# Kernel tuning notes

Hardware: AMD Instinct MI355X
Metric: run time of the kernel (lower is better)

The kernel has to match this reference:

```python
import jax, jax.numpy as jnp
import numpy as np

N_NODES = 100000
N_EDGES = 400000
N_GRAPHS = 4000
IN_DIM = 128
HID = 512
N_DESC = 200
N_CLASSES = 2


def setup_inputs() -> dict:
    key = jax.random.key(0)
    ks = jax.random.split(key, 16)
    features = jax.random.normal(ks[0], (N_NODES, IN_DIM), jnp.float32)
    descriptors = jax.random.normal(ks[1], (N_GRAPHS, N_DESC), jnp.float32)
    src = jax.random.randint(ks[2], (N_EDGES,), 0, N_NODES)
    dst = jax.random.randint(ks[3], (N_EDGES,), 0, N_NODES)
    node2graph = jnp.sort(jax.random.randint(ks[4], (N_NODES,), 0, N_GRAPHS))

    def unif(k, shape, fan_out):
        stdv = 1.0 / np.sqrt(fan_out)
        return jax.random.uniform(k, shape, jnp.float32, -stdv, stdv)

    # GCN layer params (torch init: uniform(-1/sqrt(out), 1/sqrt(out)))
    W1 = unif(ks[5], (IN_DIM, HID), HID)
    b1 = unif(ks[6], (HID,), HID)
    W2 = unif(ks[7], (HID, HID), HID)
    b2 = unif(ks[8], (HID,), HID)
    # MLP head (torch Linear default init: uniform(-1/sqrt(fan_in), ...))
    lw1 = unif(ks[9], (HID + N_DESC, 500), HID + N_DESC)
    lb1 = unif(ks[10], (500,), HID + N_DESC)
    lw2 = unif(ks[11], (500, 100), 500)
    lb2 = unif(ks[12], (100,), 500)
    cw = unif(ks[13], (100, N_CLASSES), 100)
    cb = unif(ks[14], (N_CLASSES,), 100)
    return {"features": features, "descriptors": descriptors, "src": src,
            "dst": dst, "node2graph": node2graph, "W1": W1, "b1": b1,
            "W2": W2, "b2": b2, "lw1": lw1, "lb1": lb1, "lw2": lw2,
            "lb2": lb2, "cw": cw, "cb": cb}


def reference(features, descriptors, src, dst, node2graph,
              W1, b1, W2, b2, lw1, lb1, lw2, lb2, cw, cb):
    N = features.shape[0]
    B = descriptors.shape[0]

    def gcn(h, W, b):
        hW = h @ W                                    # [N, F_out]
        # copy_src + sum: gather source features per edge, scatter-sum to dst
        agg = jax.ops.segment_sum(hW[src], dst, num_segments=N)
        return jax.nn.relu(agg + b)

    h = gcn(features, W1, b1)                         # dropout skipped (eval)
    h = gcn(h, W2, b2)

    # dgl.mean_nodes: per-graph mean over nodes
    sums = jax.ops.segment_sum(h, node2graph, num_segments=B)     # [B, HID]
    counts = jax.ops.segment_sum(jnp.ones((N,), h.dtype), node2graph,
                                 num_segments=B)
    hg = sums / jnp.maximum(counts, 1.0)[:, None]

    x = jnp.concatenate([hg, descriptors], axis=1)    # [B, HID+N_DESC]
    x = jax.nn.relu(x @ lw1 + lb1)
    x = jax.nn.relu(x @ lw2 + lb2)
    return x @ cw + cb                                # [B, n_classes]
```

## Files before the change

kernel.cpp:

```cpp
#include <hip/hip_runtime.h>
#include <hip/hip_bf16.h>

#define N_NODES  100000
#define N_EDGES  400000
#define N_GRAPHS 4000
#define IN_DIM   128
#define HID      512
#define N_DESC   200
#define N_CLASSES 2
#define MLP1_OUT 500
#define MLP2_OUT 100
#define XIN_DIM  (HID + N_DESC)
#define XIN_PAD  768

#define SCAN_CHUNK 1024
#define NCHK ((N_NODES + SCAN_CHUNK - 1) / SCAN_CHUNK)

typedef __hip_bfloat16  bf16;
typedef __hip_bfloat162 bf16x2;
typedef short s8v  __attribute__((ext_vector_type(8)));
typedef float f32x4 __attribute__((ext_vector_type(4)));

__device__ __forceinline__ float ldf(const float* p, size_t i) { return p[i]; }
__device__ __forceinline__ float ldf(const bf16* p, size_t i)  { return __bfloat162float(p[i]); }

__device__ __forceinline__ float2 ld2(const float* p, int i) { return ((const float2*)p)[i]; }
__device__ __forceinline__ float2 ld2(const bf16* p, int i)  {
    return __bfloat1622float2(((const bf16x2*)p)[i]);
}

__device__ __forceinline__ void store_out(float* p, float v) { *p = v; }
__device__ __forceinline__ void store_out(bf16* p, float v)  { *p = __float2bfloat16(v); }

__device__ __forceinline__ short f2bs(float x) {
    bf16 h = __float2bfloat16(x);
    return __builtin_bit_cast(short, h);
}

__device__ __forceinline__ void gld16(const short* g, short* l) {
    __builtin_amdgcn_global_load_lds(
        (const __attribute__((address_space(1))) unsigned int*)g,
        (__attribute__((address_space(3))) unsigned int*)l, 16, 0, 0);
}

__global__ __launch_bounds__(256)
void detect_dtype_kernel(const unsigned* __restrict__ words, unsigned nw,
                         int* __restrict__ flag)
{
    __shared__ int s_cnt;
    if (threadIdx.x == 0) s_cnt = 0;
    __syncthreads();
    const int SAMPLES = 2048;
    int sane = 0;
    for (int i = threadIdx.x; i < SAMPLES; i += 256) {
        size_t idx = (size_t)(((unsigned long long)i * 2654435761ull) % nw);
        unsigned w = words[idx];
        float f = __uint_as_float((w & 0xFFFFu) << 16);
        float a = fabsf(f);
        if (f == 0.0f || (a > 1e-8f && a < 1e8f)) sane++;
    }
    atomicAdd(&s_cnt, sane);
    __syncthreads();
    if (threadIdx.x == 0) *flag = (s_cnt * 10 > SAMPLES * 6) ? 1 : 0;
}

template<typename FT, int MODE>
__global__ __launch_bounds__(256)
void prep_weights_kernel(const FT* __restrict__ W1, const FT* __restrict__ W2,
                         const FT* __restrict__ lw1, const FT* __restrict__ lw2,
                         const FT* __restrict__ b1, const FT* __restrict__ b2,
                         const FT* __restrict__ lb1, const FT* __restrict__ lb2,
                         short* __restrict__ W1t, short* __restrict__ W2t,
                         short* __restrict__ lw1t, short* __restrict__ lw2t,
                         float* __restrict__ b1f, float* __restrict__ b2f,
                         float* __restrict__ lb1f, float* __restrict__ lb2f,
                         const int* __restrict__ flag)
{
    if (*flag != MODE) return;
    int i = blockIdx.x * 256 + threadIdx.x;
    if (i < 65536) {
        int n = i >> 7, k = i & 127;
        W1t[i] = f2bs(ldf(W1, (size_t)k * HID + n));
        return;
    }
    i -= 65536;
    if (i < 262144) {
        int n = i >> 9, k = i & 511;
        W2t[i] = f2bs(ldf(W2, (size_t)k * HID + n));
        return;
    }
    i -= 262144;
    if (i < 393216) {
        int n = i / XIN_PAD, k = i - n * XIN_PAD;
        lw1t[i] = (n < MLP1_OUT && k < XIN_DIM)
                      ? f2bs(ldf(lw1, (size_t)k * MLP1_OUT + n)) : (short)0;
        return;
    }
    i -= 393216;
    if (i < 65536) {
        int n = i >> 9, k = i & 511;
        lw2t[i] = (n < MLP2_OUT && k < MLP1_OUT)
                      ? f2bs(ldf(lw2, (size_t)k * MLP2_OUT + n)) : (short)0;
        return;
    }
    i -= 65536;
    if (i < 512) { b1f[i] = ldf(b1, i); return; }
    i -= 512;
    if (i < 512) { b2f[i] = ldf(b2, i); return; }
    i -= 512;
    if (i < 512) { lb1f[i] = (i < MLP1_OUT) ? ldf(lb1, i) : 0.f; return; }
    i -= 512;
    if (i < 128) { lb2f[i] = (i < MLP2_OUT) ? ldf(lb2, i) : 0.f; return; }
}

__global__ __launch_bounds__(256)
void deg_kernel(const int* __restrict__ dst, int* __restrict__ deg)
{
    int e = blockIdx.x * 256 + threadIdx.x;
    if (e < N_EDGES) atomicAdd(&deg[dst[e]], 1);
}

__global__ __launch_bounds__(256)
void scan_partial_kernel(const int* __restrict__ deg, int* __restrict__ part)
{
    int c = blockIdx.x, t = threadIdx.x;
    int i0 = c * SCAN_CHUNK + t * 4;
    int s = 0;
#pragma unroll
    for (int j = 0; j < 4; j++) {
        int i = i0 + j;
        if (i < N_NODES) s += deg[i];
    }
    __shared__ int red[256];
    red[t] = s;
    __syncthreads();
    for (int off = 128; off > 0; off >>= 1) {
        if (t < off) red[t] += red[t + off];
        __syncthreads();
    }
    if (t == 0) part[c] = red[0];
}

__global__ void scan_parts_kernel(int* __restrict__ part, int* __restrict__ edge_start)
{
    int run = 0;
    for (int c = 0; c < NCHK; c++) { int v = part[c]; part[c] = run; run += v; }
    edge_start[N_NODES] = run;
}

__global__ __launch_bounds__(256)
void scan_final_kernel(const int* __restrict__ deg, const int* __restrict__ part,
                       int* __restrict__ edge_start, int* __restrict__ cursor)
{
    int c = blockIdx.x, t = threadIdx.x;
    int i0 = c * SCAN_CHUNK + t * 4;
    int d[4];
    int tsum = 0;
#pragma unroll
    for (int j = 0; j < 4; j++) {
        int i = i0 + j;
        d[j] = (i < N_NODES) ? deg[i] : 0;
        tsum += d[j];
    }
    __shared__ int s[256];
    s[t] = tsum;
    __syncthreads();
    for (int off = 1; off < 256; off <<= 1) {
        int v = (t >= off) ? s[t - off] : 0;
        __syncthreads();
        s[t] += v;
        __syncthreads();
    }
    int run = part[c] + s[t] - tsum;
#pragma unroll
    for (int j = 0; j < 4; j++) {
        int i = i0 + j;
        if (i < N_NODES) { edge_start[i] = run; cursor[i] = run; run += d[j]; }
    }
}

__global__ __launch_bounds__(256)
void fill_kernel(const int* __restrict__ src, const int* __restrict__ dst,
                 int* __restrict__ cursor, int* __restrict__ csr_src)
{
    int e = blockIdx.x * 256 + threadIdx.x;
    if (e >= N_EDGES) return;
    int p = atomicAdd(&cursor[dst[e]], 1);
    csr_src[p] = src[e];
}

__global__ __launch_bounds__(256)
void gstart_kernel(const int* __restrict__ n2g, int* __restrict__ gstart)
{
    int n = blockIdx.x * 256 + threadIdx.x;
    if (n > N_NODES) return;
    if (n == N_NODES) {
        int last = n2g[N_NODES - 1];
        for (int g = last + 1; g <= N_GRAPHS; g++) gstart[g] = N_NODES;
        return;
    }
    int v = n2g[n];
    int prev = (n == 0) ? -1 : n2g[n - 1];
    for (int g = prev + 1; g <= v; g++) gstart[g] = n;
}

template<typename FT, int MODE>
__global__ __launch_bounds__(256)
void gather_feat_kernel(const FT* __restrict__ feat, const int* __restrict__ edge_start,
                        const int* __restrict__ csr_src, bf16* __restrict__ agg1,
                        const int* __restrict__ flag)
{
    if (*flag != MODE) return;
    int n = blockIdx.x * 4 + (threadIdx.x >> 6);
    if (n >= N_NODES) return;
    int lane = threadIdx.x & 63;
    int e0 = edge_start[n], e1 = edge_start[n + 1];
    float2 acc = {0.f, 0.f};
    for (int i = e0; i < e1; i++) {
        int s = csr_src[i];
        float2 f = ld2(feat + (size_t)s * IN_DIM, lane);
        acc.x += f.x; acc.y += f.y;
    }
    bf16x2 p;
    p.x = __float2bfloat16(acc.x);
    p.y = __float2bfloat16(acc.y);
    ((bf16x2*)(agg1 + (size_t)n * IN_DIM))[lane] = p;
}

__global__ __launch_bounds__(256)
void gather_h_kernel(const bf16* __restrict__ h1, const int* __restrict__ edge_start,
                     const int* __restrict__ csr_src, bf16* __restrict__ aggc)
{
    int n = blockIdx.x * 4 + (threadIdx.x >> 6);
    if (n >= N_NODES) return;
    int lane = threadIdx.x & 63;
    int e0 = edge_start[n], e1 = edge_start[n + 1];
    float acc[8];
#pragma unroll
    for (int j = 0; j < 8; j++) acc[j] = 0.f;
    for (int i = e0; i < e1; i++) {
        int s = csr_src[i];
        float4 r = ((const float4*)(h1 + (size_t)s * HID))[lane];
        const bf16x2* p = (const bf16x2*)&r;
#pragma unroll
        for (int q = 0; q < 4; q++) {
            float2 f = __bfloat1622float2(p[q]);
            acc[2 * q] += f.x; acc[2 * q + 1] += f.y;
        }
    }
    s8v s;
#pragma unroll
    for (int j = 0; j < 8; j++) s[j] = f2bs(acc[j]);
    ((float4*)(aggc + (size_t)n * HID))[lane] = __builtin_bit_cast(float4, s);
}

template<int NCT>
__global__ __launch_bounds__(256)
void mfma_gemm_kernel(const short* __restrict__ A, const short* __restrict__ Bt,
                      const float* __restrict__ biasf, bf16* __restrict__ Cout,
                      int M, int K, int nrt)
{
    __shared__ short smem[17408];
    short* As = smem;
    short* Bs = smem + 8192;
    short* Cs = smem;

    const int b  = blockIdx.x;
    const int r8 = b & 7;
    const int t  = b >> 3;
    const int x  = (t / NCT) * 8 + r8;
    const int y  = t % NCT;
    if (x >= nrt) return;
    const int row0 = x * 128;
    const int col0 = y * 128;

    const int tid  = threadIdx.x;
    const int lane = tid & 63;
    const int w    = tid >> 6;
    const int wr = w >> 1, wc = w & 1;
    const int m  = lane & 15, q = lane >> 4;

    const int dr = lane >> 3;
    const int dc = ((lane & 7) ^ dr) * 8;
    const short* ga[4];
    const short* gb[4];
    short* la[4];
    short* lb[4];
#pragma unroll
    for (int c = 0; c < 4; c++) {
        int r = (w * 4 + c) * 8 + dr;
        ga[c] = A  + (size_t)(row0 + r) * K + dc;
        gb[c] = Bt + (size_t)(col0 + r) * K + dc;
        la[c] = As + (w * 4 + c) * 512;
        lb[c] = Bs + (w * 4 + c) * 512;
    }

    const int sa = ((q ^ (m & 7)) * 8);

    f32x4 acc[4][4];
#pragma unroll
    for (int i = 0; i < 4; i++)
#pragma unroll
        for (int j = 0; j < 4; j++) acc[i][j] = {0.f, 0.f, 0.f, 0.f};

    for (int k0 = 0; k0 < K; k0 += 64) {
#pragma unroll
        for (int c = 0; c < 4; c++) gld16(ga[c], la[c]);
#pragma unroll
        for (int c = 0; c < 4; c++) gld16(gb[c], lb[c]);
#pragma unroll
        for (int c = 0; c < 4; c++) { ga[c] += 64; gb[c] += 64; }
        __syncthreads();

#pragma unroll
        for (int kq = 0; kq < 2; kq++) {
            const int so = sa ^ (kq * 32);
            s8v av[4], bv[4];
#pragma unroll
            for (int rt = 0; rt < 4; rt++)
                av[rt] = *(const s8v*)&As[(wr * 64 + rt * 16 + m) * 64 + so];
#pragma unroll
            for (int ct = 0; ct < 4; ct++)
                bv[ct] = *(const s8v*)&Bs[(wc * 64 + ct * 16 + m) * 64 + so];
#pragma unroll
            for (int rt = 0; rt < 4; rt++)
#pragma unroll
                for (int ct = 0; ct < 4; ct++)
                    acc[rt][ct] = __builtin_amdgcn_mfma_f32_16x16x32_bf16(
                        av[rt], bv[ct], acc[rt][ct], 0, 0, 0);
        }
        __syncthreads();
    }

#pragma unroll
    for (int rt = 0; rt < 4; rt++) {
#pragma unroll
        for (int ct = 0; ct < 4; ct++) {
            int lcol = wc * 64 + ct * 16 + m;
            float bv = biasf[col0 + lcol];
#pragma unroll
            for (int reg = 0; reg < 4; reg++) {
                int lrow = wr * 64 + rt * 16 + q * 4 + reg;
                float v = acc[rt][ct][reg] + bv;
                v = v > 0.f ? v : 0.f;
                Cs[lrow * 136 + lcol] = f2bs(v);
            }
        }
    }
    __syncthreads();

#pragma unroll
    for (int it = 0; it < 8; it++) {
        int idx = it * 256 + tid;
        int r = idx >> 4;
        int c = (idx & 15) * 8;
        int row = row0 + r;
        if (row < M)
            *(float4*)&Cout[(size_t)row * HID + col0 + c] =
                *(const float4*)&Cs[r * 136 + c];
    }
}

__global__ __launch_bounds__(256)
void pool_graph_kernel(const bf16* __restrict__ h2, const int* __restrict__ gstart,
                       float* __restrict__ hg)
{
    int g = blockIdx.x * 4 + (threadIdx.x >> 6);
    if (g >= N_GRAPHS) return;
    int lane = threadIdx.x & 63;
    int s0 = gstart[g], s1 = gstart[g + 1];
    float acc[8];
#pragma unroll
    for (int j = 0; j < 8; j++) acc[j] = 0.f;
    for (int n = s0; n < s1; n++) {
        float4 r = ((const float4*)(h2 + (size_t)n * HID))[lane];
        const bf16x2* p = (const bf16x2*)&r;
#pragma unroll
        for (int q = 0; q < 4; q++) {
            float2 f = __bfloat1622float2(p[q]);
            acc[2 * q] += f.x; acc[2 * q + 1] += f.y;
        }
    }
    float* orow = hg + (size_t)g * HID + lane * 8;
    ((float4*)orow)[0] = make_float4(acc[0], acc[1], acc[2], acc[3]);
    ((float4*)orow)[1] = make_float4(acc[4], acc[5], acc[6], acc[7]);
}

template<typename FT, int MODE>
__global__ __launch_bounds__(256)
void build_xin_kernel(const float* __restrict__ hg, const int* __restrict__ gstart,
                      const FT* __restrict__ desc, bf16* __restrict__ xinb,
                      const int* __restrict__ flag)
{
    if (*flag != MODE) return;
    int idx = blockIdx.x * 256 + threadIdx.x;
    if (idx >= N_GRAPHS * XIN_PAD) return;
    int g = idx / XIN_PAD;
    int c = idx - g * XIN_PAD;
    float v;
    if (c < HID) {
        float cnt = (float)(gstart[g + 1] - gstart[g]);
        v = hg[(size_t)g * HID + c] / (cnt > 1.0f ? cnt : 1.0f);
    } else if (c < XIN_DIM) {
        v = ldf(desc, (size_t)g * N_DESC + (c - HID));
    } else {
        v = 0.f;
    }
    xinb[idx] = __float2bfloat16(v);
}

template<typename FT, int MODE>
__global__ __launch_bounds__(256)
void final_layer_kernel(const bf16* __restrict__ x2b, const FT* __restrict__ cw,
                        const FT* __restrict__ cb, FT* __restrict__ out,
                        const int* __restrict__ flag)
{
    if (*flag != MODE) return;
    int i = blockIdx.x * 256 + threadIdx.x;
    if (i >= N_GRAPHS * N_CLASSES) return;
    int r = i >> 1, c = i & 1;
    float acc = ldf(cb, c);
    const bf16* x = x2b + (size_t)r * HID;
#pragma unroll 4
    for (int k = 0; k < MLP2_OUT; k++)
        acc += __bfloat162float(x[k]) * ldf(cw, k * N_CLASSES + c);
    store_out(&out[i], acc);
}

static inline size_t align_up(size_t x, size_t a) { return (x + a - 1) & ~(a - 1); }
static inline int swgrid(int nrt, int nct) { return ((nrt + 7) / 8) * 8 * nct; }

extern "C" void kernel_launch(void* const* d_in, const int* in_sizes, int n_in,
                              void* d_out, int out_size, void* d_ws, size_t ws_size,
                              hipStream_t stream)
{
    const void* features    = d_in[0];
    const void* descriptors = d_in[1];
    const int*  src         = (const int*)d_in[2];
    const int*  dst         = (const int*)d_in[3];
    const int*  node2graph  = (const int*)d_in[4];
    const void* W1          = d_in[5];
    const void* b1          = d_in[6];
    const void* W2          = d_in[7];
    const void* b2          = d_in[8];
    const void* lw1         = d_in[9];
    const void* lb1         = d_in[10];
    const void* lw2         = d_in[11];
    const void* lb2         = d_in[12];
    const void* cw          = d_in[13];
    const void* cb          = d_in[14];
    (void)in_sizes; (void)n_in; (void)out_size; (void)ws_size;

    char* ws = (char*)d_ws;
    size_t off = 0;
    bf16* agg1 = (bf16*)(ws + off);
    bf16* aggc = (bf16*)(ws + off);
    bf16* xinb = (bf16*)(ws + off);
    bf16* x1b  = (bf16*)(ws + off + (size_t)8 * 1024 * 1024);
    bf16* x2b  = (bf16*)(ws + off + (size_t)16 * 1024 * 1024);
    off = align_up(off + (size_t)N_NODES * HID * sizeof(bf16), 256);
    bf16* h1 = (bf16*)(ws + off);
    bf16* h2 = (bf16*)(ws + off);
    off = align_up(off + (size_t)N_NODES * HID * sizeof(bf16), 256);
    float* hg = (float*)(ws + off);
    off = align_up(off + (size_t)N_GRAPHS * HID * sizeof(float), 256);
    int* dflag = (int*)(ws + off);          off = align_up(off + 256, 256);
    int* edge_start = (int*)(ws + off);     off = align_up(off + (N_NODES + 1) * 4, 256);
    int* cursor = (int*)(ws + off);         off = align_up(off + N_NODES * 4, 256);
    int* csr_src = (int*)(ws + off);        off = align_up(off + N_EDGES * 4, 256);
    int* part = (int*)(ws + off);           off = align_up(off + NCHK * 4, 256);
    int* deg = (int*)(ws + off);            off = align_up(off + N_NODES * 4, 256);
    int* gstart = (int*)(ws + off);         off = align_up(off + (N_GRAPHS + 1) * 4, 256);
    short* W1t  = (short*)(ws + off);       off = align_up(off + (size_t)HID * IN_DIM * 2, 256);
    short* W2t  = (short*)(ws + off);       off = align_up(off + (size_t)HID * HID * 2, 256);
    short* lw1t = (short*)(ws + off);       off = align_up(off + (size_t)512 * XIN_PAD * 2, 256);
    short* lw2t = (short*)(ws + off);       off = align_up(off + (size_t)128 * HID * 2, 256);
    float* b1f  = (float*)(ws + off);       off = align_up(off + 512 * 4, 256);
    float* b2f  = (float*)(ws + off);       off = align_up(off + 512 * 4, 256);
    float* lb1f = (float*)(ws + off);       off = align_up(off + 512 * 4, 256);
    float* lb2f = (float*)(ws + off);       off = align_up(off + 128 * 4, 256);

    detect_dtype_kernel<<<1, 256, 0, stream>>>(
        (const unsigned*)features, (unsigned)(N_NODES * IN_DIM / 2), dflag);

    {
        int nblk = (788096 + 255) / 256;
        prep_weights_kernel<float, 0><<<nblk, 256, 0, stream>>>(
            (const float*)W1, (const float*)W2, (const float*)lw1, (const float*)lw2,
            (const float*)b1, (const float*)b2, (const float*)lb1, (const float*)lb2,
            W1t, W2t, lw1t, lw2t, b1f, b2f, lb1f, lb2f, dflag);
        prep_weights_kernel<bf16, 1><<<nblk, 256, 0, stream>>>(
            (const bf16*)W1, (const bf16*)W2, (const bf16*)lw1, (const bf16*)lw2,
            (const bf16*)b1, (const bf16*)b2, (const bf16*)lb1, (const bf16*)lb2,
            W1t, W2t, lw1t, lw2t, b1f, b2f, lb1f, lb2f, dflag);
    }

    hipMemsetAsync(deg, 0, N_NODES * 4, stream);
    deg_kernel<<<(N_EDGES + 255) / 256, 256, 0, stream>>>(dst, deg);
    scan_partial_kernel<<<NCHK, 256, 0, stream>>>(deg, part);
    scan_parts_kernel<<<1, 1, 0, stream>>>(part, edge_start);
    scan_final_kernel<<<NCHK, 256, 0, stream>>>(deg, part, edge_start, cursor);
    fill_kernel<<<(N_EDGES + 255) / 256, 256, 0, stream>>>(src, dst, cursor, csr_src);
    gstart_kernel<<<(N_NODES + 256) / 256, 256, 0, stream>>>(node2graph, gstart);

    gather_feat_kernel<float, 0><<<N_NODES / 4, 256, 0, stream>>>(
        (const float*)features, edge_start, csr_src, agg1, dflag);
    gather_feat_kernel<bf16, 1><<<N_NODES / 4, 256, 0, stream>>>(
        (const bf16*)features, edge_start, csr_src, agg1, dflag);
    {
        int nrt = (N_NODES + 127) / 128;
        mfma_gemm_kernel<4><<<swgrid(nrt, 4), 256, 0, stream>>>(
            (const short*)agg1, W1t, b1f, h1, N_NODES, IN_DIM, nrt);
    }

    gather_h_kernel<<<N_NODES / 4, 256, 0, stream>>>(h1, edge_start, csr_src, aggc);
    {
        int nrt = (N_NODES + 127) / 128;
        mfma_gemm_kernel<4><<<swgrid(nrt, 4), 256, 0, stream>>>(
            (const short*)aggc, W2t, b2f, h2, N_NODES, HID, nrt);
    }
    pool_graph_kernel<<<N_GRAPHS / 4, 256, 0, stream>>>(h2, gstart, hg);

    {
        int nthr = (N_GRAPHS * XIN_PAD + 255) / 256;
        build_xin_kernel<float, 0><<<nthr, 256, 0, stream>>>(
            hg, gstart, (const float*)descriptors, xinb, dflag);
        build_xin_kernel<bf16, 1><<<nthr, 256, 0, stream>>>(
            hg, gstart, (const bf16*)descriptors, xinb, dflag);
    }
    {
        int nrt = (N_GRAPHS + 127) / 128;
        mfma_gemm_kernel<4><<<swgrid(nrt, 4), 256, 0, stream>>>(
            (const short*)xinb, lw1t, lb1f, x1b, N_GRAPHS, XIN_PAD, nrt);
    }
    {
        int nrt = (N_GRAPHS + 127) / 128;
        mfma_gemm_kernel<1><<<swgrid(nrt, 1), 256, 0, stream>>>(
            (const short*)x1b, lw2t, lb2f, x2b, N_GRAPHS, HID, nrt);
    }
    {
        int nthr = (N_GRAPHS * N_CLASSES + 255) / 256;
        final_layer_kernel<float, 0><<<nthr, 256, 0, stream>>>(
            x2b, (const float*)cw, (const float*)cb, (float*)d_out, dflag);
        final_layer_kernel<bf16, 1><<<nthr, 256, 0, stream>>>(
            x2b, (const bf16*)cw, (const bf16*)cb, (bf16*)d_out, dflag);
    }
}
```

Measured before the change: 478.5 us.

## Merge dtype-dispatched kernel pairs, unroll gathers by four, shrink GEMM epilogue LDS

Each pair of float/bf16 kernel launches gated by a device flag becomes a single launch that branches on the flag inside the kernel. This removes four redundant launches that did nothing but exit early. The edge gathers and graph pooling loops are unrolled by four so several independent row loads are in flight per wavefront. The GEMM epilogue now writes the output tile through LDS in two 64-row halves, which cuts shared memory to 16384 shorts and may raise occupancy, at the cost of an extra barrier.

```diff
diff --git a/kernel.cpp b/kernel.cpp
--- a/kernel.cpp
+++ b/kernel.cpp
@@ -29,9 +29,6 @@
     return __bfloat1622float2(((const bf16x2*)p)[i]);
 }
 
-__device__ __forceinline__ void store_out(float* p, float v) { *p = v; }
-__device__ __forceinline__ void store_out(bf16* p, float v)  { *p = __float2bfloat16(v); }
-
 __device__ __forceinline__ short f2bs(float x) {
     bf16 h = __float2bfloat16(x);
     return __builtin_bit_cast(short, h);
@@ -64,53 +61,55 @@
     if (threadIdx.x == 0) *flag = (s_cnt * 10 > SAMPLES * 6) ? 1 : 0;
 }
 
-template<typename FT, int MODE>
-__global__ __launch_bounds__(256)
-void prep_weights_kernel(const FT* __restrict__ W1, const FT* __restrict__ W2,
-                         const FT* __restrict__ lw1, const FT* __restrict__ lw2,
-                         const FT* __restrict__ b1, const FT* __restrict__ b2,
-                         const FT* __restrict__ lb1, const FT* __restrict__ lb2,
+__global__ __launch_bounds__(256)
+void prep_weights_kernel(const void* __restrict__ W1, const void* __restrict__ W2,
+                         const void* __restrict__ lw1, const void* __restrict__ lw2,
+                         const void* __restrict__ b1, const void* __restrict__ b2,
+                         const void* __restrict__ lb1, const void* __restrict__ lb2,
                          short* __restrict__ W1t, short* __restrict__ W2t,
                          short* __restrict__ lw1t, short* __restrict__ lw2t,
                          float* __restrict__ b1f, float* __restrict__ b2f,
                          float* __restrict__ lb1f, float* __restrict__ lb2f,
                          const int* __restrict__ flag)
 {
-    if (*flag != MODE) return;
+    const int bf = *flag;
+    auto rd = [&](const void* p, size_t idx) -> float {
+        return bf ? __bfloat162float(((const bf16*)p)[idx]) : ((const float*)p)[idx];
+    };
     int i = blockIdx.x * 256 + threadIdx.x;
     if (i < 65536) {
         int n = i >> 7, k = i & 127;
-        W1t[i] = f2bs(ldf(W1, (size_t)k * HID + n));
+        W1t[i] = f2bs(rd(W1, (size_t)k * HID + n));
         return;
     }
     i -= 65536;
     if (i < 262144) {
         int n = i >> 9, k = i & 511;
-        W2t[i] = f2bs(ldf(W2, (size_t)k * HID + n));
+        W2t[i] = f2bs(rd(W2, (size_t)k * HID + n));
         return;
     }
     i -= 262144;
     if (i < 393216) {
         int n = i / XIN_PAD, k = i - n * XIN_PAD;
         lw1t[i] = (n < MLP1_OUT && k < XIN_DIM)
-                      ? f2bs(ldf(lw1, (size_t)k * MLP1_OUT + n)) : (short)0;
+                      ? f2bs(rd(lw1, (size_t)k * MLP1_OUT + n)) : (short)0;
         return;
     }
     i -= 393216;
     if (i < 65536) {
         int n = i >> 9, k = i & 511;
         lw2t[i] = (n < MLP2_OUT && k < MLP1_OUT)
-                      ? f2bs(ldf(lw2, (size_t)k * MLP2_OUT + n)) : (short)0;
+                      ? f2bs(rd(lw2, (size_t)k * MLP2_OUT + n)) : (short)0;
         return;
     }
     i -= 65536;
-    if (i < 512) { b1f[i] = ldf(b1, i); return; }
+    if (i < 512) { b1f[i] = rd(b1, i); return; }
     i -= 512;
-    if (i < 512) { b2f[i] = ldf(b2, i); return; }
+    if (i < 512) { b2f[i] = rd(b2, i); return; }
     i -= 512;
-    if (i < 512) { lb1f[i] = (i < MLP1_OUT) ? ldf(lb1, i) : 0.f; return; }
+    if (i < 512) { lb1f[i] = (i < MLP1_OUT) ? rd(lb1, i) : 0.f; return; }
     i -= 512;
-    if (i < 128) { lb2f[i] = (i < MLP2_OUT) ? ldf(lb2, i) : 0.f; return; }
+    if (i < 128) { lb2f[i] = (i < MLP2_OUT) ? rd(lb2, i) : 0.f; return; }
 }
 
 __global__ __launch_bounds__(256)
@@ -204,19 +203,29 @@
     for (int g = prev + 1; g <= v; g++) gstart[g] = n;
 }
 
-template<typename FT, int MODE>
-__global__ __launch_bounds__(256)
-void gather_feat_kernel(const FT* __restrict__ feat, const int* __restrict__ edge_start,
-                        const int* __restrict__ csr_src, bf16* __restrict__ agg1,
-                        const int* __restrict__ flag)
-{
-    if (*flag != MODE) return;
+template<typename FT>
+__device__ __forceinline__ void gather_feat_body(const FT* __restrict__ feat,
+                                                 const int* __restrict__ edge_start,
+                                                 const int* __restrict__ csr_src,
+                                                 bf16* __restrict__ agg1)
+{
     int n = blockIdx.x * 4 + (threadIdx.x >> 6);
     if (n >= N_NODES) return;
     int lane = threadIdx.x & 63;
     int e0 = edge_start[n], e1 = edge_start[n + 1];
     float2 acc = {0.f, 0.f};
-    for (int i = e0; i < e1; i++) {
+    int i = e0;
+    for (; i + 4 <= e1; i += 4) {
+        int s0 = csr_src[i], s1 = csr_src[i + 1];
+        int s2 = csr_src[i + 2], s3 = csr_src[i + 3];
+        float2 f0 = ld2(feat + (size_t)s0 * IN_DIM, lane);
+        float2 f1 = ld2(feat + (size_t)s1 * IN_DIM, lane);
+        float2 f2 = ld2(feat + (size_t)s2 * IN_DIM, lane);
+        float2 f3 = ld2(feat + (size_t)s3 * IN_DIM, lane);
+        acc.x += (f0.x + f1.x) + (f2.x + f3.x);
+        acc.y += (f0.y + f1.y) + (f2.y + f3.y);
+    }
+    for (; i < e1; i++) {
         int s = csr_src[i];
         float2 f = ld2(feat + (size_t)s * IN_DIM, lane);
         acc.x += f.x; acc.y += f.y;
@@ -225,6 +234,25 @@
     p.x = __float2bfloat16(acc.x);
     p.y = __float2bfloat16(acc.y);
     ((bf16x2*)(agg1 + (size_t)n * IN_DIM))[lane] = p;
+}
+
+__global__ __launch_bounds__(256)
+void gather_feat_kernel(const void* __restrict__ feat, const int* __restrict__ edge_start,
+                        const int* __restrict__ csr_src, bf16* __restrict__ agg1,
+                        const int* __restrict__ flag)
+{
+    if (*flag) gather_feat_body((const bf16*)feat, edge_start, csr_src, agg1);
+    else       gather_feat_body((const float*)feat, edge_start, csr_src, agg1);
+}
+
+__device__ __forceinline__ void acc8(float* acc, float4 r)
+{
+    const bf16x2* p = (const bf16x2*)&r;
+#pragma unroll
+    for (int q = 0; q < 4; q++) {
+        float2 f = __bfloat1622float2(p[q]);
+        acc[2 * q] += f.x; acc[2 * q + 1] += f.y;
+    }
 }
 
 __global__ __launch_bounds__(256)
@@ -238,15 +266,19 @@
     float acc[8];
 #pragma unroll
     for (int j = 0; j < 8; j++) acc[j] = 0.f;
-    for (int i = e0; i < e1; i++) {
+    int i = e0;
+    for (; i + 4 <= e1; i += 4) {
+        int s0 = csr_src[i], s1 = csr_src[i + 1];
+        int s2 = csr_src[i + 2], s3 = csr_src[i + 3];
+        float4 r0 = ((const float4*)(h1 + (size_t)s0 * HID))[lane];
+        float4 r1 = ((const float4*)(h1 + (size_t)s1 * HID))[lane];
+        float4 r2 = ((const float4*)(h1 + (size_t)s2 * HID))[lane];
+        float4 r3 = ((const float4*)(h1 + (size_t)s3 * HID))[lane];
+        acc8(acc, r0); acc8(acc, r1); acc8(acc, r2); acc8(acc, r3);
+    }
+    for (; i < e1; i++) {
         int s = csr_src[i];
-        float4 r = ((const float4*)(h1 + (size_t)s * HID))[lane];
-        const bf16x2* p = (const bf16x2*)&r;
-#pragma unroll
-        for (int q = 0; q < 4; q++) {
-            float2 f = __bfloat1622float2(p[q]);
-            acc[2 * q] += f.x; acc[2 * q + 1] += f.y;
-        }
+        acc8(acc, ((const float4*)(h1 + (size_t)s * HID))[lane]);
     }
     s8v s;
 #pragma unroll
@@ -260,7 +292,7 @@
                       const float* __restrict__ biasf, bf16* __restrict__ Cout,
                       int M, int K, int nrt)
 {
-    __shared__ short smem[17408];
+    __shared__ short smem[16384];
     short* As = smem;
     short* Bs = smem + 8192;
     short* Cs = smem;
@@ -333,31 +365,36 @@
     }
 
 #pragma unroll
-    for (int rt = 0; rt < 4; rt++) {
-#pragma unroll
-        for (int ct = 0; ct < 4; ct++) {
-            int lcol = wc * 64 + ct * 16 + m;
-            float bv = biasf[col0 + lcol];
-#pragma unroll
-            for (int reg = 0; reg < 4; reg++) {
-                int lrow = wr * 64 + rt * 16 + q * 4 + reg;
-                float v = acc[rt][ct][reg] + bv;
-                v = v > 0.f ? v : 0.f;
-                Cs[lrow * 136 + lcol] = f2bs(v);
+    for (int half = 0; half < 2; half++) {
+        if (half == 1) __syncthreads();
+        if (wr == half) {
+#pragma unroll
+            for (int rt = 0; rt < 4; rt++) {
+#pragma unroll
+                for (int ct = 0; ct < 4; ct++) {
+                    int lcol = wc * 64 + ct * 16 + m;
+                    float bv = biasf[col0 + lcol];
+#pragma unroll
+                    for (int reg = 0; reg < 4; reg++) {
+                        int lrow = rt * 16 + q * 4 + reg;
+                        float v = acc[rt][ct][reg] + bv;
+                        v = v > 0.f ? v : 0.f;
+                        Cs[lrow * 136 + lcol] = f2bs(v);
+                    }
+                }
             }
         }
-    }
-    __syncthreads();
-
-#pragma unroll
-    for (int it = 0; it < 8; it++) {
-        int idx = it * 256 + tid;
-        int r = idx >> 4;
-        int c = (idx & 15) * 8;
-        int row = row0 + r;
-        if (row < M)
-            *(float4*)&Cout[(size_t)row * HID + col0 + c] =
-                *(const float4*)&Cs[r * 136 + c];
+        __syncthreads();
+#pragma unroll
+        for (int it = 0; it < 4; it++) {
+            int idx = it * 256 + tid;
+            int r = idx >> 4;
+            int c = (idx & 15) * 8;
+            int row = row0 + half * 64 + r;
+            if (row < M)
+                *(float4*)&Cout[(size_t)row * HID + col0 + c] =
+                    *(const float4*)&Cs[r * 136 + c];
+        }
     }
 }
 
@@ -372,27 +409,27 @@
     float acc[8];
 #pragma unroll
     for (int j = 0; j < 8; j++) acc[j] = 0.f;
-    for (int n = s0; n < s1; n++) {
-        float4 r = ((const float4*)(h2 + (size_t)n * HID))[lane];
-        const bf16x2* p = (const bf16x2*)&r;
-#pragma unroll
-        for (int q = 0; q < 4; q++) {
-            float2 f = __bfloat1622float2(p[q]);
-            acc[2 * q] += f.x; acc[2 * q + 1] += f.y;
-        }
-    }
+    int n = s0;
+    for (; n + 4 <= s1; n += 4) {
+        float4 r0 = ((const float4*)(h2 + (size_t)(n + 0) * HID))[lane];
+        float4 r1 = ((const float4*)(h2 + (size_t)(n + 1) * HID))[lane];
+        float4 r2 = ((const float4*)(h2 + (size_t)(n + 2) * HID))[lane];
+        float4 r3 = ((const float4*)(h2 + (size_t)(n + 3) * HID))[lane];
+        acc8(acc, r0); acc8(acc, r1); acc8(acc, r2); acc8(acc, r3);
+    }
+    for (; n < s1; n++)
+        acc8(acc, ((const float4*)(h2 + (size_t)n * HID))[lane]);
     float* orow = hg + (size_t)g * HID + lane * 8;
     ((float4*)orow)[0] = make_float4(acc[0], acc[1], acc[2], acc[3]);
     ((float4*)orow)[1] = make_float4(acc[4], acc[5], acc[6], acc[7]);
 }
 
-template<typename FT, int MODE>
-__global__ __launch_bounds__(256)
-void build_xin_kernel(const float* __restrict__ hg, const int* __restrict__ gstart,
-                      const FT* __restrict__ desc, bf16* __restrict__ xinb,
-                      const int* __restrict__ flag)
-{
-    if (*flag != MODE) return;
+template<typename FT>
+__device__ __forceinline__ void build_xin_body(const float* __restrict__ hg,
+                                               const int* __restrict__ gstart,
+                                               const FT* __restrict__ desc,
+                                               bf16* __restrict__ xinb)
+{
     int idx = blockIdx.x * 256 + threadIdx.x;
     if (idx >= N_GRAPHS * XIN_PAD) return;
     int g = idx / XIN_PAD;
@@ -409,22 +446,40 @@
     xinb[idx] = __float2bfloat16(v);
 }
 
-template<typename FT, int MODE>
-__global__ __launch_bounds__(256)
-void final_layer_kernel(const bf16* __restrict__ x2b, const FT* __restrict__ cw,
-                        const FT* __restrict__ cb, FT* __restrict__ out,
-                        const int* __restrict__ flag)
-{
-    if (*flag != MODE) return;
+__global__ __launch_bounds__(256)
+void build_xin_kernel(const float* __restrict__ hg, const int* __restrict__ gstart,
+                      const void* __restrict__ desc, bf16* __restrict__ xinb,
+                      const int* __restrict__ flag)
+{
+    if (*flag) build_xin_body(hg, gstart, (const bf16*)desc, xinb);
+    else       build_xin_body(hg, gstart, (const float*)desc, xinb);
+}
+
+template<typename FT>
+__device__ __forceinline__ void final_layer_body(const bf16* __restrict__ x2b,
+                                                 const FT* __restrict__ cw,
+                                                 const FT* __restrict__ cb,
+                                                 FT* __restrict__ out)
+{
     int i = blockIdx.x * 256 + threadIdx.x;
     if (i >= N_GRAPHS * N_CLASSES) return;
     int r = i >> 1, c = i & 1;
     float acc = ldf(cb, c);
-    const bf16* x = x2b + (size_t)r * HID;
+    const bf16* xrow = x2b + (size_t)r * HID;
 #pragma unroll 4
     for (int k = 0; k < MLP2_OUT; k++)
-        acc += __bfloat162float(x[k]) * ldf(cw, k * N_CLASSES + c);
-    store_out(&out[i], acc);
+        acc += __bfloat162float(xrow[k]) * ldf(cw, k * N_CLASSES + c);
+    if constexpr (sizeof(FT) == 2) out[i] = __float2bfloat16(acc);
+    else                           out[i] = acc;
+}
+
+__global__ __launch_bounds__(256)
+void final_layer_kernel(const bf16* __restrict__ x2b, const void* __restrict__ cw,
+                        const void* __restrict__ cb, void* __restrict__ out,
+                        const int* __restrict__ flag)
+{
+    if (*flag) final_layer_body(x2b, (const bf16*)cw, (const bf16*)cb, (bf16*)out);
+    else       final_layer_body(x2b, (const float*)cw, (const float*)cb, (float*)out);
 }
 
 static inline size_t align_up(size_t x, size_t a) { return (x + a - 1) & ~(a - 1); }
@@ -483,17 +538,9 @@
     detect_dtype_kernel<<<1, 256, 0, stream>>>(
         (const unsigned*)features, (unsigned)(N_NODES * IN_DIM / 2), dflag);
 
-    {
-        int nblk = (788096 + 255) / 256;
-        prep_weights_kernel<float, 0><<<nblk, 256, 0, stream>>>(
-            (const float*)W1, (const float*)W2, (const float*)lw1, (const float*)lw2,
-            (const float*)b1, (const float*)b2, (const float*)lb1, (const float*)lb2,
-            W1t, W2t, lw1t, lw2t, b1f, b2f, lb1f, lb2f, dflag);
-        prep_weights_kernel<bf16, 1><<<nblk, 256, 0, stream>>>(
-            (const bf16*)W1, (const bf16*)W2, (const bf16*)lw1, (const bf16*)lw2,
-            (const bf16*)b1, (const bf16*)b2, (const bf16*)lb1, (const bf16*)lb2,
-            W1t, W2t, lw1t, lw2t, b1f, b2f, lb1f, lb2f, dflag);
-    }
+    prep_weights_kernel<<<(788096 + 255) / 256, 256, 0, stream>>>(
+        W1, W2, lw1, lw2, b1, b2, lb1, lb2,
+        W1t, W2t, lw1t, lw2t, b1f, b2f, lb1f, lb2f, dflag);
 
     hipMemsetAsync(deg, 0, N_NODES * 4, stream);
     deg_kernel<<<(N_EDGES + 255) / 256, 256, 0, stream>>>(dst, deg);
@@ -503,10 +550,8 @@
     fill_kernel<<<(N_EDGES + 255) / 256, 256, 0, stream>>>(src, dst, cursor, csr_src);
     gstart_kernel<<<(N_NODES + 256) / 256, 256, 0, stream>>>(node2graph, gstart);
 
-    gather_feat_kernel<float, 0><<<N_NODES / 4, 256, 0, stream>>>(
-        (const float*)features, edge_start, csr_src, agg1, dflag);
-    gather_feat_kernel<bf16, 1><<<N_NODES / 4, 256, 0, stream>>>(
-        (const bf16*)features, edge_start, csr_src, agg1, dflag);
+    gather_feat_kernel<<<N_NODES / 4, 256, 0, stream>>>(
+        features, edge_start, csr_src, agg1, dflag);
     {
         int nrt = (N_NODES + 127) / 128;
         mfma_gemm_kernel<4><<<swgrid(nrt, 4), 256, 0, stream>>>(
@@ -521,13 +566,8 @@
     }
     pool_graph_kernel<<<N_GRAPHS / 4, 256, 0, stream>>>(h2, gstart, hg);
 
-    {
-        int nthr = (N_GRAPHS * XIN_PAD + 255) / 256;
-        build_xin_kernel<float, 0><<<nthr, 256, 0, stream>>>(
-            hg, gstart, (const float*)descriptors, xinb, dflag);
-        build_xin_kernel<bf16, 1><<<nthr, 256, 0, stream>>>(
-            hg, gstart, (const bf16*)descriptors, xinb, dflag);
-    }
+    build_xin_kernel<<<(N_GRAPHS * XIN_PAD + 255) / 256, 256, 0, stream>>>(
+        hg, gstart, descriptors, xinb, dflag);
     {
         int nrt = (N_GRAPHS + 127) / 128;
         mfma_gemm_kernel<4><<<swgrid(nrt, 4), 256, 0, stream>>>(
@@ -538,11 +578,6 @@
         mfma_gemm_kernel<1><<<swgrid(nrt, 1), 256, 0, stream>>>(
             (const short*)x1b, lw2t, lb2f, x2b, N_GRAPHS, HID, nrt);
     }
-    {
-        int nthr = (N_GRAPHS * N_CLASSES + 255) / 256;
-        final_layer_kernel<float, 0><<<nthr, 256, 0, stream>>>(
-            x2b, (const float*)cw, (const float*)cb, (float*)d_out, dflag);
-        final_layer_kernel<bf16, 1><<<nthr, 256, 0, stream>>>(
-            x2b, (const bf16*)cw, (const bf16*)cb, (bf16*)d_out, dflag);
-    }
-}
+    final_layer_kernel<<<(N_GRAPHS * N_CLASSES + 255) / 256, 256, 0, stream>>>(
+        x2b, cw, cb, d_out, dflag);
+}
```

Result: no change. 482.1 us (+0.8%).
